# Performance work log

Measured on AMD Instinct MI355X. Metric: run time of the kernel, lower is better.

## Reference

```python
import jax, jax.numpy as jnp
import numpy as np

B, N, D, S, ITERS = 32, 4096, 256, 7, 3
EPS_LN = 1e-5

def _ln(x, g, b):
    m = jnp.mean(x, axis=-1, keepdims=True)
    v = jnp.mean((x - m) ** 2, axis=-1, keepdims=True)
    return g * (x - m) * jax.lax.rsqrt(v + EPS_LN) + b

def setup_inputs() -> dict:
    key = jax.random.key(0)
    ks = jax.random.split(key, 16)
    w = lambda k, shape: (jax.random.normal(k, shape, jnp.float32) * 0.02)
    return {
        "inputs": jax.random.normal(ks[0], (B, N, D), jnp.float32),
        "noise": jax.random.normal(ks[1], (B, S, D), jnp.float32),
        "ln_in_g": jnp.ones((D,), jnp.float32), "ln_in_b": jnp.zeros((D,), jnp.float32),
        "ln_slots_g": jnp.ones((D,), jnp.float32), "ln_slots_b": jnp.zeros((D,), jnp.float32),
        "ln_mlp_g": jnp.ones((D,), jnp.float32), "ln_mlp_b": jnp.zeros((D,), jnp.float32),
        "slots_mu": w(ks[2], (1, 1, D)),
        "slots_sigma": jnp.ones((1, 1, D), jnp.float32),
        "wq": w(ks[3], (D, D)), "bq": jnp.zeros((D,), jnp.float32),
        "wk": w(ks[4], (D, D)), "bk": jnp.zeros((D,), jnp.float32),
        "wv": w(ks[5], (D, D)), "bv": jnp.zeros((D,), jnp.float32),
        "w_ih": w(ks[6], (3 * D, D)), "b_ih": jnp.zeros((3 * D,), jnp.float32),
        "w_hh": w(ks[7], (3 * D, D)), "b_hh": jnp.zeros((3 * D,), jnp.float32),
        "w1": w(ks[8], (2 * D, D)), "b1": jnp.zeros((2 * D,), jnp.float32),
        "w2": w(ks[9], (D, 2 * D)), "b2": jnp.zeros((D,), jnp.float32),
    }

def reference(inputs, noise, ln_in_g, ln_in_b, ln_slots_g, ln_slots_b, ln_mlp_g, ln_mlp_b,
              slots_mu, slots_sigma, wq, bq, wk, bk, wv, bv,
              w_ih, b_ih, w_hh, b_hh, w1, b1, w2, b2):
    x = _ln(inputs, ln_in_g, ln_in_b)                      # [B,N,D]
    sigma = jax.nn.softplus(slots_sigma)
    slots = slots_mu + sigma * noise                       # [B,S,D]
    k = x @ wk.T + bk                                      # [B,N,D]
    v = x @ wv.T + bv                                      # [B,N,D]
    scale = D ** -0.5
    attn = None
    for _ in range(ITERS):
        slots_prev = slots
        q = _ln(slots, ln_slots_g, ln_slots_b) @ wq.T + bq  # [B,S,D]
        logits = jnp.einsum('bsd,bnd->bsn', q, k) * scale   # [B,S,N]
        attn = jax.nn.softmax(logits, axis=1) + 1e-8        # softmax over slots
        attn = attn / jnp.sum(attn, axis=-1, keepdims=True)
        updates = jnp.einsum('bsn,bnd->bsd', attn, v)       # [B,S,D]
        # GRUCell(updates, slots_prev), torch gate order (r, z, n)
        gi = updates @ w_ih.T + b_ih                        # [B,S,3D]
        gh = slots_prev @ w_hh.T + b_hh
        i_r, i_z, i_n = jnp.split(gi, 3, axis=-1)
        h_r, h_z, h_n = jnp.split(gh, 3, axis=-1)
        r = jax.nn.sigmoid(i_r + h_r)
        z = jax.nn.sigmoid(i_z + h_z)
        n = jnp.tanh(i_n + r * h_n)
        slots = (1.0 - z) * n + z * slots_prev
        h = jax.nn.relu(_ln(slots, ln_mlp_g, ln_mlp_b) @ w1.T + b1)
        slots = slots + h @ w2.T + b2
    return slots, jnp.swapaxes(attn, 1, 2)                 # [B,S,D], [B,N,S]
```

## Files before the change

kernel.cpp:

```cpp
#include <hip/hip_runtime.h>
#include <stdint.h>

typedef unsigned short u16;
typedef unsigned int u32;
typedef float f32x4 __attribute__((ext_vector_type(4)));
typedef short short8 __attribute__((ext_vector_type(8)));

#define NBAT 32
#define NSEQ 4096
#define ND 256
#define NSLOT 7
#define NCHUNK 64

__device__ __forceinline__ u32 bf16rne(float f){
  u32 u = __float_as_uint(f);
  u = u + 0x7FFFu + ((u >> 16) & 1u);
  return u >> 16;
}
__device__ __forceinline__ u32 packbf(float a, float b){
  return (bf16rne(a) & 0xFFFFu) | (bf16rne(b) << 16);
}
__device__ __forceinline__ float bflo(u32 u){ return __uint_as_float(u << 16); }
__device__ __forceinline__ float bfhi(u32 u){ return __uint_as_float(u & 0xFFFF0000u); }

__device__ __forceinline__ void gld16(void* lds, const void* g){
  __builtin_amdgcn_global_load_lds(
      (const __attribute__((address_space(1))) u32*)g,
      (__attribute__((address_space(3))) u32*)lds, 16, 0, 0);
}

__global__ __launch_bounds__(256) void k_prep(
    const float* __restrict__ wk, const float* __restrict__ wv,
    const float* __restrict__ bk, const float* __restrict__ bv,
    const float* __restrict__ mu, const float* __restrict__ sig,
    const float* __restrict__ noise,
    const float* __restrict__ w_ih, const float* __restrict__ b_ih,
    const float* __restrict__ w_hh, const float* __restrict__ b_hh,
    const float* __restrict__ w1, const float* __restrict__ w2,
    const float* __restrict__ wq,
    u16* __restrict__ Wkv, float* __restrict__ biaskv, float* __restrict__ slots,
    u16* __restrict__ Wg, u16* __restrict__ w1b, u16* __restrict__ w2b,
    u16* __restrict__ wqb, float* __restrict__ bg){
  const int bid = blockIdx.x, t = threadIdx.x;
  if (bid < 512){
    const float* src = (bid < 256) ? (wk + (size_t)bid*256) : (wv + (size_t)(bid-256)*256);
    Wkv[(size_t)bid*256 + t] = (u16)bf16rne(src[t]);
  } else if (bid == 512){
    biaskv[t] = bk[t];
    biaskv[256 + t] = bv[t];
  } else if (bid < 737){
    int r = bid - 513;
    float sp = logf(1.f + expf(sig[t]));
    slots[(size_t)r*256 + t] = mu[t] + sp * noise[(size_t)r*256 + t];
  } else if (bid < 1761){
    int j = bid - 737;
    u16 a, b;
    if (j < 512){ a = (u16)bf16rne(w_ih[(size_t)j*256 + t]); b = (u16)bf16rne(w_hh[(size_t)j*256 + t]); }
    else if (j < 768){ a = (u16)bf16rne(w_ih[(size_t)j*256 + t]); b = 0; }
    else { a = 0; b = (u16)bf16rne(w_hh[(size_t)(j-256)*256 + t]); }
    Wg[(size_t)j*512 + t] = a;
    Wg[(size_t)j*512 + 256 + t] = b;
  } else if (bid < 2273){
    int j = bid - 1761;
    w1b[(size_t)j*256 + t] = (u16)bf16rne(w1[(size_t)j*256 + t]);
  } else if (bid < 2529){
    int j = bid - 2273;
    w2b[(size_t)j*512 + t]       = (u16)bf16rne(w2[(size_t)j*512 + t]);
    w2b[(size_t)j*512 + 256 + t] = (u16)bf16rne(w2[(size_t)j*512 + 256 + t]);
  } else if (bid < 2785){
    int j = bid - 2529;
    wqb[(size_t)j*256 + t] = (u16)bf16rne(wq[(size_t)j*256 + t]);
  } else {
#pragma unroll
    for (int ii = 0; ii < 4; ++ii){
      int j = ii*256 + t;
      float v;
      if (j < 512) v = b_ih[j] + b_hh[j];
      else if (j < 768) v = b_ih[j];
      else v = b_hh[j - 256];
      bg[j] = v;
    }
  }
}

__global__ __launch_bounds__(256) void k_ln_in(
    const float* __restrict__ x, const float* __restrict__ g, const float* __restrict__ b,
    u16* __restrict__ xo){
  const int row = blockIdx.x*4 + (threadIdx.x >> 6);
  const int lane = threadIdx.x & 63;
  const f32x4 v = *(const f32x4*)(x + (size_t)row*ND + lane*4);
  float s  = v[0]+v[1]+v[2]+v[3];
  float s2 = v[0]*v[0]+v[1]*v[1]+v[2]*v[2]+v[3]*v[3];
#pragma unroll
  for (int m = 1; m < 64; m <<= 1){ s += __shfl_xor(s, m); s2 += __shfl_xor(s2, m); }
  const float mean = s * (1.f/256.f);
  const float var  = s2 * (1.f/256.f) - mean*mean;
  const float rstd = rsqrtf(var + 1e-5f);
  const f32x4 gg = *(const f32x4*)(g + lane*4);
  const f32x4 bb = *(const f32x4*)(b + lane*4);
  float y0 = (v[0]-mean)*rstd*gg[0] + bb[0];
  float y1 = (v[1]-mean)*rstd*gg[1] + bb[1];
  float y2 = (v[2]-mean)*rstd*gg[2] + bb[2];
  float y3 = (v[3]-mean)*rstd*gg[3] + bb[3];
  uint2 o; o.x = packbf(y0, y1); o.y = packbf(y2, y3);
  *(uint2*)(xo + (size_t)row*ND + lane*4) = o;
}

__global__ __launch_bounds__(256) void k_gemm_kv(
    const u16* __restrict__ X, const u16* __restrict__ W,
    const float* __restrict__ biaskv, u16* __restrict__ kv){
  __shared__ __align__(16) u16 At[128*64];
  const int bid = blockIdx.x;
  const int swz = ((bid & 7) << 9) + (bid >> 3);
  const int mb = swz >> 2, nb = swz & 3;
  const int tid = threadIdx.x, w = tid >> 6, lane = tid & 63;
  const int wm = w >> 1, wn = w & 1;
  const int l15 = lane & 15, g = lane >> 4;
  f32x4 acc[4][4];
#pragma unroll
  for (int a = 0; a < 4; ++a)
#pragma unroll
    for (int c = 0; c < 4; ++c) acc[a][c] = (f32x4){0.f,0.f,0.f,0.f};

  const int cl = lane & 7;
  const u16* wbase = W + ((size_t)(nb*128 + wn*64 + l15))*256;
  for (int kt = 0; kt < 4; ++kt){
    short8 wf[2][4];
#pragma unroll
    for (int kk = 0; kk < 2; ++kk)
#pragma unroll
      for (int wi = 0; wi < 4; ++wi)
        wf[kk][wi] = *(const short8*)(wbase + (size_t)wi*16*256 + kt*64 + (kk*4 + g)*8);
    __syncthreads();
#pragma unroll
    for (int i = 0; i < 4; ++i){
      int R = w*32 + i*8 + (lane >> 3);
      int c = cl ^ (R & 7);
      gld16(&At[(w*32 + i*8)*64], X + ((size_t)(mb*128 + R))*256 + kt*64 + c*8);
    }
    __syncthreads();
#pragma unroll
    for (int kk = 0; kk < 2; ++kk){
      short8 xf[4];
#pragma unroll
      for (int xi = 0; xi < 4; ++xi){
        int r = wm*64 + xi*16 + l15;
        int ch = (kk*4 + g) ^ (r & 7);
        xf[xi] = *(const short8*)&At[r*64 + ch*8];
      }
#pragma unroll
      for (int xi = 0; xi < 4; ++xi)
#pragma unroll
        for (int wi = 0; wi < 4; ++wi)
          acc[xi][wi] = __builtin_amdgcn_mfma_f32_16x16x32_bf16(wf[kk][wi], xf[xi], acc[xi][wi], 0, 0, 0);
    }
  }
  f32x4 bias[4];
#pragma unroll
  for (int wi = 0; wi < 4; ++wi)
    bias[wi] = *(const f32x4*)(biaskv + nb*128 + wn*64 + wi*16 + g*4);
#pragma unroll
  for (int xi = 0; xi < 4; ++xi){
    size_t m = (size_t)mb*128 + wm*64 + xi*16 + l15;
    u16* dst = kv + m*512 + nb*128 + wn*64 + g*4;
#pragma unroll
    for (int wi = 0; wi < 4; ++wi){
      f32x4 c = acc[xi][wi];
      uint2 o;
      o.x = packbf(c[0] + bias[wi][0], c[1] + bias[wi][1]);
      o.y = packbf(c[2] + bias[wi][2], c[3] + bias[wi][3]);
      *(uint2*)(dst + wi*16) = o;
    }
  }
}

template<int MODE>
__global__ __launch_bounds__(256) void k_gemm_s(
    const u16* __restrict__ A, const u16* __restrict__ W,
    const float* __restrict__ bias, int nkt,
    float* __restrict__ outf, u16* __restrict__ outb,
    const float* __restrict__ snew, float* __restrict__ out2, int last){
  __shared__ __align__(16) u16 At[2][128*64];
  __shared__ __align__(16) u16 Bt[2][128*64];
  const int nb = blockIdx.x, mb = blockIdx.y;
  const int tid = threadIdx.x, w = tid >> 6, lane = tid & 63;
  const int wm = w >> 1, wn = w & 1;
  const size_t K = (size_t)nkt * 64;
  f32x4 acc[4][4];
#pragma unroll
  for (int a = 0; a < 4; ++a)
#pragma unroll
    for (int c = 0; c < 4; ++c) acc[a][c] = (f32x4){0.f,0.f,0.f,0.f};

  const int cl = lane & 7;
#define STAGE_S(buf, kt)                                                         \
  {                                                                              \
    _Pragma("unroll")                                                            \
    for (int i = 0; i < 4; ++i){                                                 \
      int R = w*32 + i*8 + (lane >> 3);                                          \
      int c = cl ^ (R & 7);                                                      \
      gld16(&At[buf][(w*32 + i*8)*64], A + ((size_t)(mb*128 + R))*K + (kt)*64 + c*8); \
      gld16(&Bt[buf][(w*32 + i*8)*64], W + ((size_t)(nb*128 + R))*K + (kt)*64 + c*8); \
    }                                                                            \
  }
  STAGE_S(0, 0);
  __syncthreads();
  for (int kt = 0; kt < nkt; ++kt){
    const int cur = kt & 1;
    if (kt < nkt - 1) STAGE_S(cur ^ 1, kt + 1);
#pragma unroll
    for (int kk = 0; kk < 2; ++kk){
      short8 xf[4], wf[4];
#pragma unroll
      for (int xi = 0; xi < 4; ++xi){
        int r = wm*64 + xi*16 + (lane & 15);
        int ch = (kk*4 + (lane >> 4)) ^ (r & 7);
        xf[xi] = *(const short8*)&At[cur][r*64 + ch*8];
      }
#pragma unroll
      for (int wi = 0; wi < 4; ++wi){
        int r = wn*64 + wi*16 + (lane & 15);
        int ch = (kk*4 + (lane >> 4)) ^ (r & 7);
        wf[wi] = *(const short8*)&Bt[cur][r*64 + ch*8];
      }
#pragma unroll
      for (int xi = 0; xi < 4; ++xi)
#pragma unroll
        for (int wi = 0; wi < 4; ++wi)
          acc[xi][wi] = __builtin_amdgcn_mfma_f32_16x16x32_bf16(wf[wi], xf[xi], acc[xi][wi], 0, 0, 0);
    }
    __syncthreads();
  }
#undef STAGE_S
  const int LDO = (MODE == 0) ? 1024 : ((MODE == 1) ? 512 : 256);
  f32x4 b4[4];
#pragma unroll
  for (int wi = 0; wi < 4; ++wi)
    b4[wi] = *(const f32x4*)(bias + nb*128 + wn*64 + wi*16 + (lane >> 4)*4);
#pragma unroll
  for (int xi = 0; xi < 4; ++xi){
    const int m = mb*128 + wm*64 + xi*16 + (lane & 15);
    const int colb = nb*128 + wn*64 + (lane >> 4)*4;
#pragma unroll
    for (int wi = 0; wi < 4; ++wi){
      const int col = colb + wi*16;
      f32x4 c = acc[xi][wi] + b4[wi];
      if (MODE == 0){
        *(f32x4*)(outf + (size_t)m*LDO + col) = c;
      } else if (MODE == 1){
        uint2 o;
        o.x = packbf(fmaxf(c[0],0.f), fmaxf(c[1],0.f));
        o.y = packbf(fmaxf(c[2],0.f), fmaxf(c[3],0.f));
        *(uint2*)(outb + (size_t)m*LDO + col) = o;
      } else if (MODE == 2){
        if (m < 224){
          const f32x4 s4 = *(const f32x4*)(snew + (size_t)m*256 + col);
          f32x4 o = c + s4;
          *(f32x4*)(outf + (size_t)m*LDO + col) = o;
          if (last) *(f32x4*)(out2 + (size_t)m*LDO + col) = o;
        }
      } else {
        uint2 o;
        o.x = packbf(c[0]*0.09016844f, c[1]*0.09016844f);
        o.y = packbf(c[2]*0.09016844f, c[3]*0.09016844f);
        *(uint2*)(outb + (size_t)m*LDO + col) = o;
      }
    }
  }
}

__global__ __launch_bounds__(256) void k_attn(
    const u16* __restrict__ kv, const u16* __restrict__ qb,
    float* __restrict__ attn_out, float* __restrict__ pacc, float* __restrict__ pw){
  __shared__ __align__(16) float accbuf[4][7][256];
  __shared__ __align__(16) float p_lds[4][16][8];
  __shared__ float wsum_lds[4][8];
  const int chunk = blockIdx.x, b = blockIdx.y;
  const int tid = threadIdx.x, w = tid >> 6, lane = tid & 63;
  const int l15 = lane & 15, g = lane >> 4, hi = lane >> 5;
  const size_t bbase = (size_t)b*NSEQ;
  const int nr0 = chunk*64 + w*16;

  short8 qf[8];
  {
    const u16* qrow = qb + ((size_t)b*7 + l15)*256;
#pragma unroll
    for (int ks = 0; ks < 8; ++ks)
      qf[ks] = *(const short8*)(qrow + (ks*4 + g)*8);
  }
  f32x4 z = {0.f,0.f,0.f,0.f};
#pragma unroll
  for (int ks = 0; ks < 8; ++ks){
    const short8 kf = *(const short8*)(kv + (bbase + nr0 + l15)*512 + (ks*4 + g)*8);
    z = __builtin_amdgcn_mfma_f32_16x16x32_bf16(qf[ks], kf, z, 0, 0, 0);
  }
  float zz[4];
#pragma unroll
  for (int j = 0; j < 4; ++j){
    const int s = g*4 + j;
    zz[j] = (s < 7) ? z[j] : -3.0e38f;
  }
  float mx = fmaxf(fmaxf(zz[0], zz[1]), fmaxf(zz[2], zz[3]));
  mx = fmaxf(mx, __shfl_xor(mx, 16));
  float p[4], psum = 0.f;
#pragma unroll
  for (int j = 0; j < 4; ++j){ p[j] = exp2f(zz[j] - mx); psum += p[j]; }
  psum += __shfl_xor(psum, 16);
  const float rs = 1.f / psum;
#pragma unroll
  for (int j = 0; j < 4; ++j) p[j] = fmaf(p[j], rs, 1e-8f);
  float wloc[4] = {0.f,0.f,0.f,0.f};
  if (lane < 32){
    *(f32x4*)&p_lds[w][l15][g*4] = (f32x4){p[0], p[1], p[2], p[3]};
    const size_t arow = (bbase + nr0 + l15)*7;
#pragma unroll
    for (int j = 0; j < 4; ++j){
      const int s = g*4 + j;
      if (s < 7){ attn_out[arow + s] = p[j]; wloc[j] = p[j]; }
    }
  }
  __syncthreads();
  float acc[7][4];
#pragma unroll
  for (int s = 0; s < 7; ++s){ acc[s][0]=acc[s][1]=acc[s][2]=acc[s][3]=0.f; }
#pragma unroll
  for (int it = 0; it < 8; ++it){
    const int rm = it*2 + hi, ro = it*2 + (1 - hi);
    const uint2 va = *(const uint2*)(kv + (bbase + nr0 + rm)*512 + 256 + (size_t)lane*4);
    const uint2 vb = *(const uint2*)(kv + (bbase + nr0 + ro)*512 + 256 + (size_t)lane*4);
    const f32x4 pm0 = *(const f32x4*)&p_lds[w][rm][0];
    const f32x4 pm1 = *(const f32x4*)&p_lds[w][rm][4];
    const f32x4 po0 = *(const f32x4*)&p_lds[w][ro][0];
    const f32x4 po1 = *(const f32x4*)&p_lds[w][ro][4];
    const float pm[7] = {pm0[0],pm0[1],pm0[2],pm0[3],pm1[0],pm1[1],pm1[2]};
    const float po[7] = {po0[0],po0[1],po0[2],po0[3],po1[0],po1[1],po1[2]};
    const float vm0=bflo(va.x), vm1=bfhi(va.x), vm2=bflo(va.y), vm3=bfhi(va.y);
    const float vo0=bflo(vb.x), vo1=bfhi(vb.x), vo2=bflo(vb.y), vo3=bfhi(vb.y);
#pragma unroll
    for (int s = 0; s < 7; ++s){
      acc[s][0] = fmaf(pm[s], vm0, fmaf(po[s], vo0, acc[s][0]));
      acc[s][1] = fmaf(pm[s], vm1, fmaf(po[s], vo1, acc[s][1]));
      acc[s][2] = fmaf(pm[s], vm2, fmaf(po[s], vo2, acc[s][2]));
      acc[s][3] = fmaf(pm[s], vm3, fmaf(po[s], vo3, acc[s][3]));
    }
  }
#pragma unroll
  for (int m = 1; m < 16; m <<= 1){
#pragma unroll
    for (int j = 0; j < 4; ++j) wloc[j] += __shfl_xor(wloc[j], m);
  }
  if (lane < 32 && l15 == 0){
#pragma unroll
    for (int j = 0; j < 4; ++j) wsum_lds[w][g*4 + j] = wloc[j];
  }
  __syncthreads();
#pragma unroll
  for (int s = 0; s < 7; ++s)
    *(f32x4*)&accbuf[w][s][lane*4] = (f32x4){acc[s][0], acc[s][1], acc[s][2], acc[s][3]};
  __syncthreads();
#pragma unroll
  for (int s = 0; s < 7; ++s){
    float sum = accbuf[0][s][tid] + accbuf[1][s][tid] + accbuf[2][s][tid] + accbuf[3][s][tid];
    pacc[((size_t)chunk*NBAT + b)*(NSLOT*256) + s*256 + tid] = sum;
  }
  if (tid < 7)
    pw[((size_t)chunk*NBAT + b)*NSLOT + tid] =
        wsum_lds[0][tid] + wsum_lds[1][tid] + wsum_lds[2][tid] + wsum_lds[3][tid];
}

__global__ __launch_bounds__(256) void k_slotA(
    const float* __restrict__ pacc, const float* __restrict__ pw,
    const float* __restrict__ slots, u16* __restrict__ A2, float* __restrict__ wsum){
  __shared__ float pwb[NCHUNK];
  const int r = blockIdx.x, t = threadIdx.x;
  if (r >= 224){
    A2[(size_t)r*512 + t] = 0;
    A2[(size_t)r*512 + 256 + t] = 0;
    return;
  }
  if (t < NCHUNK) pwb[t] = pw[(size_t)t*224 + r];
  float u = 0.f;
#pragma unroll 8
  for (int c = 0; c < NCHUNK; ++c) u += pacc[(size_t)c*57344 + (size_t)r*256 + t];
  __syncthreads();
  float wst = 0.f;
#pragma unroll
  for (int c = 0; c < NCHUNK; ++c) wst += pwb[c];
  if (t == 0) wsum[r] = wst;
  A2[(size_t)r*512 + t] = (u16)bf16rne(u / wst);
  A2[(size_t)r*512 + 256 + t] = (u16)bf16rne(slots[(size_t)r*256 + t]);
}

__global__ __launch_bounds__(256) void k_slotB(
    const float* __restrict__ gates, const float* __restrict__ slots,
    const float* __restrict__ gm, const float* __restrict__ bm,
    float* __restrict__ snew, u16* __restrict__ lnm){
  __shared__ float red[8];
  const int r = blockIdx.x, t = threadIdx.x;
  if (r >= 224){ lnm[(size_t)r*256 + t] = 0; return; }
  const float g0  = gates[(size_t)r*1024 + t];
  const float g1  = gates[(size_t)r*1024 + 256 + t];
  const float gin = gates[(size_t)r*1024 + 512 + t];
  const float ghn = gates[(size_t)r*1024 + 768 + t];
  const float spv = slots[(size_t)r*256 + t];
  const float rr = 1.f/(1.f + __expf(-g0));
  const float zz = 1.f/(1.f + __expf(-g1));
  float xx = gin + rr*ghn;
  xx = fminf(fmaxf(xx, -15.f), 15.f);
  const float e2 = __expf(2.f*xx);
  const float nn = (e2 - 1.f)/(e2 + 1.f);
  const float sp = (1.f - zz)*nn + zz*spv;
  snew[(size_t)r*256 + t] = sp;
  float s = sp, s2 = sp*sp;
#pragma unroll
  for (int m = 1; m < 64; m <<= 1){ s += __shfl_xor(s, m); s2 += __shfl_xor(s2, m); }
  if ((t & 63) == 0){ red[t >> 6] = s; red[4 + (t >> 6)] = s2; }
  __syncthreads();
  const float ssum = red[0]+red[1]+red[2]+red[3];
  const float qsum = red[4]+red[5]+red[6]+red[7];
  const float mean = ssum*(1.f/256.f);
  const float var  = qsum*(1.f/256.f) - mean*mean;
  const float rstd = rsqrtf(var + 1e-5f);
  lnm[(size_t)r*256 + t] = (u16)bf16rne((sp - mean)*rstd*gm[t] + bm[t]);
}

__global__ __launch_bounds__(256) void k_lnq(
    const float* __restrict__ slots, const float* __restrict__ g, const float* __restrict__ b,
    u16* __restrict__ lnq){
  __shared__ float red[8];
  const int r = blockIdx.x, t = threadIdx.x;
  if (r >= 224){ lnq[(size_t)r*256 + t] = 0; return; }
  const float x = slots[(size_t)r*256 + t];
  float s = x, s2 = x*x;
#pragma unroll
  for (int m = 1; m < 64; m <<= 1){ s += __shfl_xor(s, m); s2 += __shfl_xor(s2, m); }
  if ((t & 63) == 0){ red[t >> 6] = s; red[4 + (t >> 6)] = s2; }
  __syncthreads();
  const float ssum = red[0]+red[1]+red[2]+red[3];
  const float qsum = red[4]+red[5]+red[6]+red[7];
  const float mean = ssum*(1.f/256.f);
  const float var  = qsum*(1.f/256.f) - mean*mean;
  const float rstd = rsqrtf(var + 1e-5f);
  lnq[(size_t)r*256 + t] = (u16)bf16rne((x - mean)*rstd*g[t] + b[t]);
}

__global__ __launch_bounds__(256) void k_norm(
    float* __restrict__ attn, const float* __restrict__ wsum_tot){
  size_t i = (size_t)blockIdx.x*256 + threadIdx.x;
  int s = (int)(i % 7);
  int b = (int)(i / (NSEQ*7));
  attn[i] = attn[i] / wsum_tot[b*7 + s];
}

extern "C" void kernel_launch(void* const* d_in, const int* in_sizes, int n_in,
                              void* d_out, int out_size, void* d_ws, size_t ws_size,
                              hipStream_t stream){
  (void)in_sizes; (void)n_in; (void)out_size; (void)ws_size;
  const float* inputs  = (const float*)d_in[0];
  const float* noise   = (const float*)d_in[1];
  const float* ln_in_g = (const float*)d_in[2];
  const float* ln_in_b = (const float*)d_in[3];
  const float* ln_sl_g = (const float*)d_in[4];
  const float* ln_sl_b = (const float*)d_in[5];
  const float* ln_ml_g = (const float*)d_in[6];
  const float* ln_ml_b = (const float*)d_in[7];
  const float* mu      = (const float*)d_in[8];
  const float* sig     = (const float*)d_in[9];
  const float* wq      = (const float*)d_in[10];
  const float* bq      = (const float*)d_in[11];
  const float* wk      = (const float*)d_in[12];
  const float* bk      = (const float*)d_in[13];
  const float* wv      = (const float*)d_in[14];
  const float* bv      = (const float*)d_in[15];
  const float* w_ih    = (const float*)d_in[16];
  const float* b_ih    = (const float*)d_in[17];
  const float* w_hh    = (const float*)d_in[18];
  const float* b_hh    = (const float*)d_in[19];
  const float* w1      = (const float*)d_in[20];
  const float* b1      = (const float*)d_in[21];
  const float* w2      = (const float*)d_in[22];
  const float* b2      = (const float*)d_in[23];

  char* ws = (char*)d_ws;
  u16*   x_bf   = (u16*)(ws);
  u16*   kv     = (u16*)(ws + 67108864);
  char*  paccch = ws + 201326592;
  float* pacc   = (float*)paccch;
  u16*   Wkv    = (u16*)(ws + 216006656);
  u16*   qeffb  = (u16*)(ws + 216268800);
  float* slots  = (float*)(ws + 216530944);
  float* pw     = (float*)(ws + 216760320);
  float* biaskv = (float*)(ws + 216817664);
  float* wsum   = (float*)(ws + 216819712);
  u16*   A2     = (u16*)(ws + 216820736);
  u16*   Wg     = (u16*)(ws + 217082880);
  u16*   w1b    = (u16*)(ws + 218131456);
  u16*   w2b    = (u16*)(ws + 218393600);
  u16*   wqb    = (u16*)(ws + 218655744);
  float* bg     = (float*)(ws + 218786816);

  float* gates  = (float*)(paccch);
  u16*   hb     = (u16*)(paccch + 1048576);
  u16*   lnm    = (u16*)(paccch + 1310720);
  u16*   lnq    = (u16*)(paccch + 1441792);
  float* snew   = (float*)(paccch + 1572864);

  float* out_slots = (float*)d_out;
  float* attn = (float*)d_out + 57344;

  k_prep<<<2786, 256, 0, stream>>>(wk, wv, bk, bv, mu, sig, noise,
                                   w_ih, b_ih, w_hh, b_hh, w1, w2, wq,
                                   Wkv, biaskv, slots, Wg, w1b, w2b, wqb, bg);
  k_ln_in<<<32768, 256, 0, stream>>>(inputs, ln_in_g, ln_in_b, x_bf);
  k_gemm_kv<<<4096, 256, 0, stream>>>(x_bf, Wkv, biaskv, kv);
  for (int i = 0; i < 3; ++i){
    const int last = (i == 2) ? 1 : 0;
    k_lnq<<<256, 256, 0, stream>>>(slots, ln_sl_g, ln_sl_b, lnq);
    k_gemm_s<3><<<dim3(2, 2), 256, 0, stream>>>(lnq, wqb, bq, 4, nullptr, qeffb, nullptr, nullptr, 0);
    k_attn<<<dim3(NCHUNK, 32), 256, 0, stream>>>(kv, qeffb, attn, pacc, pw);
    k_slotA<<<256, 256, 0, stream>>>(pacc, pw, slots, A2, wsum);
    k_gemm_s<0><<<dim3(8, 2), 256, 0, stream>>>(A2, Wg, bg, 8, gates, nullptr, nullptr, nullptr, 0);
    k_slotB<<<256, 256, 0, stream>>>(gates, slots, ln_ml_g, ln_ml_b, snew, lnm);
    k_gemm_s<1><<<dim3(4, 2), 256, 0, stream>>>(lnm, w1b, b1, 4, nullptr, hb, nullptr, nullptr, 0);
    k_gemm_s<2><<<dim3(2, 2), 256, 0, stream>>>(hb, w2b, b2, 8, slots, nullptr, snew, out_slots, last);
  }
  k_norm<<<3584, 256, 0, stream>>>(attn, wsum);
}
```

Baseline: 397.9 us.

## Fuse slot LayerNorm with Q projection and stage KV weights via LDS

Replaces the separate slot LayerNorm kernel and the small MFMA Q-projection GEMM with one per-row kernel. It normalizes the slot row, then computes the scaled q row by wave-reduced dot products against the bf16 wq, which removes one launch and the lnq round-trip per iteration. In the K/V projection GEMM, weight fragments are now loaded cooperatively into a swizzled LDS tile alongside the activation tile, rather than read by each wave directly from global memory into registers. That adds an LDS buffer and a trailing barrier per k-step. The padded query rows beyond 224 are no longer written.

```diff
diff --git a/kernel.cpp b/kernel.cpp
--- a/kernel.cpp
+++ b/kernel.cpp
@@ -110,12 +110,12 @@
     const u16* __restrict__ X, const u16* __restrict__ W,
     const float* __restrict__ biaskv, u16* __restrict__ kv){
   __shared__ __align__(16) u16 At[128*64];
+  __shared__ __align__(16) u16 Bt[128*64];
   const int bid = blockIdx.x;
   const int swz = ((bid & 7) << 9) + (bid >> 3);
   const int mb = swz >> 2, nb = swz & 3;
   const int tid = threadIdx.x, w = tid >> 6, lane = tid & 63;
   const int wm = w >> 1, wn = w & 1;
-  const int l15 = lane & 15, g = lane >> 4;
   f32x4 acc[4][4];
 #pragma unroll
   for (int a = 0; a < 4; ++a)
@@ -123,46 +123,46 @@
     for (int c = 0; c < 4; ++c) acc[a][c] = (f32x4){0.f,0.f,0.f,0.f};
 
   const int cl = lane & 7;
-  const u16* wbase = W + ((size_t)(nb*128 + wn*64 + l15))*256;
   for (int kt = 0; kt < 4; ++kt){
-    short8 wf[2][4];
-#pragma unroll
-    for (int kk = 0; kk < 2; ++kk)
-#pragma unroll
-      for (int wi = 0; wi < 4; ++wi)
-        wf[kk][wi] = *(const short8*)(wbase + (size_t)wi*16*256 + kt*64 + (kk*4 + g)*8);
-    __syncthreads();
 #pragma unroll
     for (int i = 0; i < 4; ++i){
       int R = w*32 + i*8 + (lane >> 3);
       int c = cl ^ (R & 7);
       gld16(&At[(w*32 + i*8)*64], X + ((size_t)(mb*128 + R))*256 + kt*64 + c*8);
+      gld16(&Bt[(w*32 + i*8)*64], W + ((size_t)(nb*128 + R))*256 + kt*64 + c*8);
     }
     __syncthreads();
 #pragma unroll
     for (int kk = 0; kk < 2; ++kk){
-      short8 xf[4];
+      short8 xf[4], wf[4];
 #pragma unroll
       for (int xi = 0; xi < 4; ++xi){
-        int r = wm*64 + xi*16 + l15;
-        int ch = (kk*4 + g) ^ (r & 7);
+        int r = wm*64 + xi*16 + (lane & 15);
+        int ch = (kk*4 + (lane >> 4)) ^ (r & 7);
         xf[xi] = *(const short8*)&At[r*64 + ch*8];
       }
 #pragma unroll
+      for (int wi = 0; wi < 4; ++wi){
+        int r = wn*64 + wi*16 + (lane & 15);
+        int ch = (kk*4 + (lane >> 4)) ^ (r & 7);
+        wf[wi] = *(const short8*)&Bt[r*64 + ch*8];
+      }
+#pragma unroll
       for (int xi = 0; xi < 4; ++xi)
 #pragma unroll
         for (int wi = 0; wi < 4; ++wi)
-          acc[xi][wi] = __builtin_amdgcn_mfma_f32_16x16x32_bf16(wf[kk][wi], xf[xi], acc[xi][wi], 0, 0, 0);
-    }
+          acc[xi][wi] = __builtin_amdgcn_mfma_f32_16x16x32_bf16(wf[wi], xf[xi], acc[xi][wi], 0, 0, 0);
+    }
+    __syncthreads();
   }
   f32x4 bias[4];
 #pragma unroll
   for (int wi = 0; wi < 4; ++wi)
-    bias[wi] = *(const f32x4*)(biaskv + nb*128 + wn*64 + wi*16 + g*4);
+    bias[wi] = *(const f32x4*)(biaskv + nb*128 + wn*64 + wi*16 + (lane >> 4)*4);
 #pragma unroll
   for (int xi = 0; xi < 4; ++xi){
-    size_t m = (size_t)mb*128 + wm*64 + xi*16 + l15;
-    u16* dst = kv + m*512 + nb*128 + wn*64 + g*4;
+    size_t m = (size_t)mb*128 + wm*64 + xi*16 + (lane & 15);
+    u16* dst = kv + m*512 + nb*128 + wn*64 + (lane >> 4)*4;
 #pragma unroll
     for (int wi = 0; wi < 4; ++wi){
       f32x4 c = acc[xi][wi];
@@ -259,12 +259,50 @@
           *(f32x4*)(outf + (size_t)m*LDO + col) = o;
           if (last) *(f32x4*)(out2 + (size_t)m*LDO + col) = o;
         }
-      } else {
-        uint2 o;
-        o.x = packbf(c[0]*0.09016844f, c[1]*0.09016844f);
-        o.y = packbf(c[2]*0.09016844f, c[3]*0.09016844f);
-        *(uint2*)(outb + (size_t)m*LDO + col) = o;
       }
+    }
+  }
+}
+
+__global__ __launch_bounds__(256) void k_q(
+    const float* __restrict__ slots, const float* __restrict__ g, const float* __restrict__ b,
+    const u16* __restrict__ wqb, const float* __restrict__ bq, u16* __restrict__ qeffb){
+  __shared__ float lnv[256];
+  __shared__ float red[8];
+  const int r = blockIdx.x, t = threadIdx.x, w = t >> 6, lane = t & 63;
+  const float x = slots[(size_t)r*256 + t];
+  float s = x, s2 = x*x;
+#pragma unroll
+  for (int m = 1; m < 64; m <<= 1){ s += __shfl_xor(s, m); s2 += __shfl_xor(s2, m); }
+  if ((t & 63) == 0){ red[t >> 6] = s; red[4 + (t >> 6)] = s2; }
+  __syncthreads();
+  const float ssum = red[0]+red[1]+red[2]+red[3];
+  const float qsum = red[4]+red[5]+red[6]+red[7];
+  const float mean = ssum*(1.f/256.f);
+  const float var  = qsum*(1.f/256.f) - mean*mean;
+  const float rstd = rsqrtf(var + 1e-5f);
+  lnv[t] = (x - mean)*rstd*g[t] + b[t];
+  __syncthreads();
+  const f32x4 l4 = *(const f32x4*)&lnv[lane*4];
+  for (int jj = 0; jj < 64; jj += 8){
+    float sv[8];
+#pragma unroll
+    for (int u8 = 0; u8 < 8; ++u8){
+      const int j = w*64 + jj + u8;
+      const uint2 wr = *(const uint2*)(wqb + (size_t)j*256 + lane*4);
+      float d = l4[0]*bflo(wr.x);
+      d = fmaf(l4[1], bfhi(wr.x), d);
+      d = fmaf(l4[2], bflo(wr.y), d);
+      d = fmaf(l4[3], bfhi(wr.y), d);
+#pragma unroll
+      for (int m = 1; m < 64; m <<= 1) d += __shfl_xor(d, m);
+      sv[u8] = d;
+    }
+#pragma unroll
+    for (int u8 = 0; u8 < 8; ++u8){
+      const int j = w*64 + jj + u8;
+      if (lane == u8)
+        qeffb[(size_t)r*256 + j] = (u16)bf16rne((sv[u8] + bq[j]) * 0.09016844f);
     }
   }
 }
@@ -422,26 +460,6 @@
   const float var  = qsum*(1.f/256.f) - mean*mean;
   const float rstd = rsqrtf(var + 1e-5f);
   lnm[(size_t)r*256 + t] = (u16)bf16rne((sp - mean)*rstd*gm[t] + bm[t]);
-}
-
-__global__ __launch_bounds__(256) void k_lnq(
-    const float* __restrict__ slots, const float* __restrict__ g, const float* __restrict__ b,
-    u16* __restrict__ lnq){
-  __shared__ float red[8];
-  const int r = blockIdx.x, t = threadIdx.x;
-  if (r >= 224){ lnq[(size_t)r*256 + t] = 0; return; }
-  const float x = slots[(size_t)r*256 + t];
-  float s = x, s2 = x*x;
-#pragma unroll
-  for (int m = 1; m < 64; m <<= 1){ s += __shfl_xor(s, m); s2 += __shfl_xor(s2, m); }
-  if ((t & 63) == 0){ red[t >> 6] = s; red[4 + (t >> 6)] = s2; }
-  __syncthreads();
-  const float ssum = red[0]+red[1]+red[2]+red[3];
-  const float qsum = red[4]+red[5]+red[6]+red[7];
-  const float mean = ssum*(1.f/256.f);
-  const float var  = qsum*(1.f/256.f) - mean*mean;
-  const float rstd = rsqrtf(var + 1e-5f);
-  lnq[(size_t)r*256 + t] = (u16)bf16rne((x - mean)*rstd*g[t] + b[t]);
 }
 
 __global__ __launch_bounds__(256) void k_norm(
@@ -502,7 +520,6 @@
   float* gates  = (float*)(paccch);
   u16*   hb     = (u16*)(paccch + 1048576);
   u16*   lnm    = (u16*)(paccch + 1310720);
-  u16*   lnq    = (u16*)(paccch + 1441792);
   float* snew   = (float*)(paccch + 1572864);
 
   float* out_slots = (float*)d_out;
@@ -515,8 +532,7 @@
   k_gemm_kv<<<4096, 256, 0, stream>>>(x_bf, Wkv, biaskv, kv);
   for (int i = 0; i < 3; ++i){
     const int last = (i == 2) ? 1 : 0;
-    k_lnq<<<256, 256, 0, stream>>>(slots, ln_sl_g, ln_sl_b, lnq);
-    k_gemm_s<3><<<dim3(2, 2), 256, 0, stream>>>(lnq, wqb, bq, 4, nullptr, qeffb, nullptr, nullptr, 0);
+    k_q<<<224, 256, 0, stream>>>(slots, ln_sl_g, ln_sl_b, wqb, bq, qeffb);
     k_attn<<<dim3(NCHUNK, 32), 256, 0, stream>>>(kv, qeffb, attn, pacc, pw);
     k_slotA<<<256, 256, 0, stream>>>(pacc, pw, slots, A2, wsum);
     k_gemm_s<0><<<dim3(8, 2), 256, 0, stream>>>(A2, Wg, bg, 8, gates, nullptr, nullptr, nullptr, 0);
```

Measured after the change: 369.1 us. 1.08x faster.
